# Kernel optimization log

Measured on AMD Instinct MI355X. Metric: run time of the kernel, lower is better.

The kernel has to match this reference:

```python
import jax, jax.numpy as jnp
import numpy as np

BETA = 8.0  # cfg.memory.beta (inverse temperature)
EPS = 1e-12  # matches F.normalize default eps


def _l2_normalize(x):
    return x / jnp.maximum(jnp.linalg.norm(x, axis=-1, keepdims=True), EPS)


def setup_inputs() -> dict:
    key = jax.random.key(0)
    k1, k2, k3 = jax.random.split(key, 3)
    embeddings = jax.random.normal(k1, (1024, 128), dtype=jnp.float32)   # queries [B, D]
    keys = jax.random.normal(k2, (100000, 128), dtype=jnp.float32)       # stored patterns [N, D]
    labels = jax.random.randint(k3, (100000,), 0, 1000)                  # class per stored pattern [N]
    return {"embeddings": embeddings, "keys": keys, "labels": labels, "n_classes": 1000}


def reference(embeddings, keys, labels, n_classes):
    # store(): keys normalized (normalize_keys=True); values = one_hot(labels)
    k = _l2_normalize(keys)
    # query(): normalize queries, cosine sims, softmax(beta*sims), weighted value sum
    q = _l2_normalize(embeddings)
    sims = q @ k.T                                   # [B, N]
    weights = jax.nn.softmax(BETA * sims, axis=-1)   # [B, N]
    # weights @ one_hot(labels, C) == segment-sum of weights by key label (same math,
    # avoids materializing the dense [N, C] one-hot value matrix)
    out = jax.ops.segment_sum(weights.T, labels, num_segments=n_classes).T  # [B, C]
    return out
```

## Files before the change

kernel.cpp:

```cpp
#include <hip/hip_runtime.h>
#include <math.h>

typedef _Float16 f16;
typedef _Float16 f16x8 __attribute__((ext_vector_type(8)));
typedef float    f32x16 __attribute__((ext_vector_type(16)));
typedef unsigned int uint;
typedef unsigned short u16;

#define B_Q     1024
#define DIM     128
#define N_KEYS  100000
#define NPAD    102400
#define NGP     (NPAD / 32)
#define GPC     8
#define NCHUNK  (NGP / GPC)
#define N_CLS   1000
#define QSCALE  11.541560327111707f
#define NH      128
#define QGRP    (B_Q / 32)

__global__ void k_hist(const int* __restrict__ labels, uint* __restrict__ hist128) {
    __shared__ uint lh[N_CLS];
    for (int i = threadIdx.x; i < N_CLS; i += blockDim.x) lh[i] = 0;
    __syncthreads();
    const int stride = gridDim.x * blockDim.x;
    for (int i = blockIdx.x * blockDim.x + threadIdx.x; i < N_KEYS; i += stride)
        atomicAdd(&lh[labels[i]], 1u);
    __syncthreads();
    for (int i = threadIdx.x; i < N_CLS; i += blockDim.x)
        hist128[blockIdx.x * N_CLS + i] = lh[i];
}

__global__ void k_scan(const uint* __restrict__ hist128, uint* __restrict__ cursor) {
    __shared__ uint s[1024];
    const int t = threadIdx.x;
    uint v = 0;
    if (t < N_CLS)
        for (int b = 0; b < NH; ++b) v += hist128[b * N_CLS + t];
    s[t] = v; __syncthreads();
    for (int o = 1; o < 1024; o <<= 1) {
        const uint x = (t >= o) ? s[t - o] : 0u;
        __syncthreads();
        s[t] += x;
        __syncthreads();
    }
    if (t < N_CLS) cursor[t] = s[t] - v;
}

__global__ void k_perm(const int* __restrict__ labels, uint* __restrict__ cursor,
                       int* __restrict__ src, u16* __restrict__ kcls) {
    const int n = blockIdx.x * blockDim.x + threadIdx.x;
    if (n >= NPAD) return;
    if (n < N_KEYS) {
        const int lab = labels[n];
        const int pos = (int)atomicAdd(&cursor[lab], 1u);
        src[pos]  = n;
        kcls[pos] = (u16)lab;
    } else {
        src[n]  = -1;
        kcls[n] = (u16)N_CLS;
    }
}

__global__ __launch_bounds__(256)
void k_gather(const float* __restrict__ qm, const float* __restrict__ km,
              const int* __restrict__ src, f16* __restrict__ kf2,
              f16* __restrict__ qf2) {
    __shared__ float ssq[8][32];
    __shared__ float scale[32];
    const int g = blockIdx.x;
    const int t = threadIdx.x;
    const int r = t & 31;
    const int p = t >> 5;
    const bool isq = g >= NGP;

    const float* srow;
    if (isq) srow = qm + (size_t)((g - NGP) * 32 + r) * DIM;
    else {
        const int sr = src[g * 32 + r];
        srow = (sr >= 0) ? km + (size_t)sr * DIM : nullptr;
    }

    float4 v[4];
    float ss = 0.0f;
    if (srow) {
        #pragma unroll
        for (int i = 0; i < 4; ++i) {
            v[i] = *(const float4*)(srow + p * 16 + i * 4);
            ss += v[i].x * v[i].x + v[i].y * v[i].y
                + v[i].z * v[i].z + v[i].w * v[i].w;
        }
    } else {
        #pragma unroll
        for (int i = 0; i < 4; ++i) v[i] = float4{0.f, 0.f, 0.f, 0.f};
    }
    ssq[p][r] = ss;
    __syncthreads();
    if (t < 32) {
        float s = 0.0f;
        #pragma unroll
        for (int i = 0; i < 8; ++i) s += ssq[i][t];
        scale[t] = (isq ? QSCALE : 1.0f) / fmaxf(sqrtf(s), 1e-12f);
    }
    __syncthreads();
    const float sc = scale[r];

    const float f[16] = {v[0].x, v[0].y, v[0].z, v[0].w,
                         v[1].x, v[1].y, v[1].z, v[1].w,
                         v[2].x, v[2].y, v[2].z, v[2].w,
                         v[3].x, v[3].y, v[3].z, v[3].w};
    f16x8 h0, h1;
    #pragma unroll
    for (int j = 0; j < 8; ++j) {
        h0[j] = (f16)(f[j]     * sc);
        h1[j] = (f16)(f[j + 8] * sc);
    }
    f16* dst = isq ? qf2 + (size_t)(g - NGP) * 4096
                   : kf2 + (size_t)g * 4096;
    *(f16x8*)(dst + p * 512 +       r * 8) = h0;
    *(f16x8*)(dst + p * 512 + 256 + r * 8) = h1;
}

#define ZFLOATS ((N_CLS + 2) * B_Q)
__global__ void k_meta(const u16* __restrict__ kcls, int* __restrict__ meta,
                       float* __restrict__ out_t) {
    const int nt = gridDim.x * blockDim.x;
    const float4 z = {0.0f, 0.0f, 0.0f, 0.0f};
    for (int i = blockIdx.x * blockDim.x + threadIdx.x; i < ZFLOATS / 4; i += nt)
        ((float4*)out_t)[i] = z;

    const int gid  = blockIdx.x * blockDim.x + threadIdx.x;
    const int g    = gid >> 6;
    const int lane = threadIdx.x & 63;
    if (g >= NGP) return;
    const int  cl = kcls[g * 32 + (lane & 31)];
    const int  ca = __shfl(cl, 0);
    const uint dm = (uint)(__ballot(cl != ca) & 0xffffffffull);
    const int  split = dm ? (__ffs(dm) - 1) : 32;
    const int  cb = (split < 32) ? __shfl(cl, split) : ca;
    if (lane == 0) meta[g] = ca | (cb << 11) | (split << 22);
}

#define FLUSH2(C) {                                                           \
        const float v0 = racc0 + __shfl_xor(racc0, 32);                       \
        const float v1 = racc1 + __shfl_xor(racc1, 32);                       \
        if ((C) != N_CLS) { tot0 += racc0; tot1 += racc1; }                   \
        if (lhi == 0) {                                                       \
            atomicAdd(&out_t[(size_t)(C) * B_Q + q00 + l31], v0);             \
            atomicAdd(&out_t[(size_t)(C) * B_Q + q01 + l31], v1);             \
        }                                                                     \
    }

#define LOADK(DST, I) {                                                       \
        const f16* _kb = kf2 + (size_t)(g0 + (I)) * 4096 + lane * 8;          \
        _Pragma("unroll")                                                     \
        for (int kk = 0; kk < 8; ++kk) DST[kk] = *(const f16x8*)(_kb + kk * 512); \
    }

#define BODY(KB, I) {                                                         \
        const int m     = __shfl(mv, (I));       \
        const int ca    = m & 0x7FF;                                          \
        const int cb    = (m >> 11) & 0x7FF;                                  \
        const int split = m >> 22;                                            \
        f32x16 c0 = {}, c1 = {};                                              \
        _Pragma("unroll")                                                     \
        for (int kk = 0; kk < 8; ++kk) {                                      \
            c0 = __builtin_amdgcn_mfma_f32_32x32x16_f16(KB[kk], Q0[kk], c0, 0, 0, 0); \
            c1 = __builtin_amdgcn_mfma_f32_32x32x16_f16(KB[kk], Q1[kk], c1, 0, 0, 0); \
        }                                                                     \
        if (ca != cur) {                                                      \
            if (cur >= 0) FLUSH2(cur);                                        \
            racc0 = 0.0f; racc1 = 0.0f;                                       \
            cur = ca;                                                         \
        }                                                                     \
        if (split == 32) {                                                    \
            float ga = 0.f, gb = 0.f, gc = 0.f, gd = 0.f;                     \
            _Pragma("unroll")                                                 \
            for (int r = 0; r < 16; r += 2) {                                 \
                ga += __builtin_amdgcn_exp2f(c0[r]);                          \
                gb += __builtin_amdgcn_exp2f(c0[r + 1]);                      \
                gc += __builtin_amdgcn_exp2f(c1[r]);                          \
                gd += __builtin_amdgcn_exp2f(c1[r + 1]);                      \
            }                                                                 \
            racc0 += ga + gb;                                                 \
            racc1 += gc + gd;                                                 \
        } else {                                                              \
            float ga = 0.f, gb = 0.f, gc = 0.f, gd = 0.f;                     \
            float ha = 0.f, hb = 0.f, hc = 0.f, hd = 0.f;                     \
            _Pragma("unroll")                                                 \
            for (int r = 0; r < 16; r += 2) {                                 \
                const int  kr0 = ((r & 3) + 8 * (r >> 2)) + lhi4;             \
                const int  kr1 = (((r + 1) & 3) + 8 * ((r + 1) >> 2)) + lhi4; \
                const float e0  = __builtin_amdgcn_exp2f(c0[r]);              \
                const float e0b = __builtin_amdgcn_exp2f(c0[r + 1]);          \
                const float e1  = __builtin_amdgcn_exp2f(c1[r]);              \
                const float e1b = __builtin_amdgcn_exp2f(c1[r + 1]);          \
                const bool inA0 = kr0 < split;                                \
                const bool inA1 = kr1 < split;                                \
                ga += inA0 ? e0  : 0.0f;  ha += inA0 ? 0.0f : e0;             \
                gb += inA1 ? e0b : 0.0f;  hb += inA1 ? 0.0f : e0b;            \
                gc += inA0 ? e1  : 0.0f;  hc += inA0 ? 0.0f : e1;             \
                gd += inA1 ? e1b : 0.0f;  hd += inA1 ? 0.0f : e1b;            \
            }                                                                 \
            racc0 += ga + gb;                                                 \
            racc1 += gc + gd;                                                 \
            FLUSH2(cur);                                                      \
            racc0 = ha + hb;                                                  \
            racc1 = hc + hd;                                                  \
            cur = cb;                                                         \
        }                                                                     \
    }

__global__ __launch_bounds__(64)
void class_gemm7(const f16* __restrict__ kf2, const f16* __restrict__ qf2,
                 const int* __restrict__ meta, float* __restrict__ out_t,
                 float* __restrict__ qtot) {
    const int lane = threadIdx.x & 63;
    const int l31  = lane & 31;
    const int lhi  = lane >> 5;
    const int lhi4 = lhi << 2;

    const int b     = blockIdx.x;
    const int xcd   = b & 7;
    const int u     = b >> 3;
    const int chunk = xcd * (NCHUNK / 8) + (u >> 4);
    const int qquad = (u >> 2) & 3;
    const int wsub  = u & 3;
    const int g0    = chunk * GPC;

    f16x8 Q0[8], Q1[8];
    {
        const f16* qa = qf2 + (size_t)(qquad * 8 + wsub * 2) * 4096 + lane * 8;
        #pragma unroll
        for (int kk = 0; kk < 8; ++kk) {
            Q0[kk] = *(const f16x8*)(qa + kk * 512);
            Q1[kk] = *(const f16x8*)(qa + 4096 + kk * 512);
        }
    }
    const int q00 = qquad * 256 + wsub * 64;
    const int q01 = q00 + 32;

    const int mv = meta[g0 + (lane & (GPC - 1))];

    float racc0 = 0.0f, racc1 = 0.0f;
    float tot0  = 0.0f, tot1  = 0.0f;
    int cur = -1;

    f16x8 K0[8], K1[8];
    LOADK(K0, 0);
    #pragma unroll
    for (int ii = 0; ii < GPC / 2; ++ii) {
        { const int i = 2 * ii;     if (i + 1 < GPC) LOADK(K1, i + 1); BODY(K0, i); }
        { const int i = 2 * ii + 1; if (i + 1 < GPC) LOADK(K0, i + 1); BODY(K1, i); }
    }
    if (cur >= 0) FLUSH2(cur);

    {
        const float t0 = tot0 + __shfl_xor(tot0, 32);
        const float t1 = tot1 + __shfl_xor(tot1, 32);
        if (lhi == 0) {
            atomicAdd(&qtot[q00 + l31], t0);
            atomicAdd(&qtot[q01 + l31], t1);
        }
    }
}

__global__ __launch_bounds__(256)
void k_norm_t(const float* __restrict__ out_t, const float* __restrict__ qtot,
              float* __restrict__ out) {
    __shared__ float tile[64 * 65];
    __shared__ float invq[64];
    const int tid  = threadIdx.x;
    const int w    = tid >> 6;
    const int lane = tid & 63;
    const int q0   = blockIdx.x * 64;
    const int c0   = blockIdx.y * 64;

    if (tid < 64) invq[tid] = 1.0f / qtot[q0 + tid];

    #pragma unroll
    for (int i = 0; i < 16; ++i) {
        const int cidx = c0 + w * 16 + i;
        const float v = (cidx < N_CLS) ? out_t[(size_t)cidx * B_Q + q0 + lane] : 0.0f;
        tile[lane * 65 + w * 16 + i] = v;
    }
    __syncthreads();
    #pragma unroll
    for (int j = 0; j < 16; ++j) {
        const int r    = w * 16 + j;
        const int cidx = c0 + lane;
        if (cidx < N_CLS)
            out[(size_t)(q0 + r) * N_CLS + cidx] = tile[r * 65 + lane] * invq[r];
    }
}

extern "C" void kernel_launch(void* const* d_in, const int* in_sizes, int n_in,
                              void* d_out, int out_size, void* d_ws, size_t ws_size,
                              hipStream_t stream) {
    const float* qm     = (const float*)d_in[0];
    const float* km     = (const float*)d_in[1];
    const int*   labels = (const int*)d_in[2];
    float* out = (float*)d_out;

    char* p = (char*)d_ws;
    f16*   kf2     = (f16*)p;   p += (size_t)NPAD * DIM * 2;
    f16*   qf2     = (f16*)p;   p += (size_t)B_Q * DIM * 2;
    float* out_t   = (float*)p; p += (size_t)N_CLS * B_Q * 4;
    float* sink    = (float*)p; p += (size_t)B_Q * 4;
    float* qtot    = (float*)p; p += (size_t)B_Q * 4;
    uint*  cursor  = (uint*)p;  p += N_CLS * 4;
    u16*   kcls    = (u16*)p;   p += (size_t)NPAD * 2;
    int*   meta    = (int*)p;   p += (size_t)NGP * 4;
    int*   src     = (int*)p;   p += (size_t)NPAD * 4;
    (void)sink;
    uint*  hist128 = (uint*)out_t;

    hipLaunchKernelGGL(k_hist, dim3(NH), dim3(256), 0, stream, labels, hist128);
    hipLaunchKernelGGL(k_scan, dim3(1), dim3(1024), 0, stream, hist128, cursor);
    hipLaunchKernelGGL(k_perm, dim3(NPAD / 256), dim3(256), 0, stream,
                       labels, cursor, src, kcls);
    hipLaunchKernelGGL(k_gather, dim3(NGP + QGRP), dim3(256), 0, stream,
                       qm, km, src, kf2, qf2);
    hipLaunchKernelGGL(k_meta, dim3((NGP * 64 + 255) / 256), dim3(256), 0, stream,
                       kcls, meta, out_t);

    hipLaunchKernelGGL(class_gemm7, dim3(16 * NCHUNK), dim3(64), 0, stream,
                       kf2, qf2, meta, out_t, qtot);

    hipLaunchKernelGGL(k_norm_t, dim3(B_Q / 64, (N_CLS + 63) / 64), dim3(256), 0, stream,
                       out_t, qtot, out);
}
```

Before: 101.6 us.

## Fuse meta/zeroing into gather, wave-shuffle scan, and double GPC per block

Removes the separate k_meta launch by folding output zeroing and per-group class metadata computation into k_gather. Rewrites the single-block scan to use wave-level shuffle prefix sums instead of a shared-memory Hillis-Steele loop with many barriers. Doubles key groups per GEMM block (halving grid size) and switches the main loop to non-unrolled, reducing launch overhead and meta reloads at the cost of less parallelism and a possibly weaker software pipeline.

```diff
diff --git a/kernel.cpp b/kernel.cpp
--- a/kernel.cpp
+++ b/kernel.cpp
@@ -12,12 +12,13 @@
 #define N_KEYS  100000
 #define NPAD    102400
 #define NGP     (NPAD / 32)
-#define GPC     8
+#define GPC     16
 #define NCHUNK  (NGP / GPC)
 #define N_CLS   1000
 #define QSCALE  11.541560327111707f
 #define NH      128
 #define QGRP    (B_Q / 32)
+#define ZFLOATS ((N_CLS + 2) * B_Q)
 
 __global__ void k_hist(const int* __restrict__ labels, uint* __restrict__ hist128) {
     __shared__ uint lh[N_CLS];
@@ -31,20 +32,34 @@
         hist128[blockIdx.x * N_CLS + i] = lh[i];
 }
 
-__global__ void k_scan(const uint* __restrict__ hist128, uint* __restrict__ cursor) {
-    __shared__ uint s[1024];
+__global__ __launch_bounds__(1024)
+void k_scan(const uint* __restrict__ hist128, uint* __restrict__ cursor) {
+    __shared__ uint wtot[16];
     const int t = threadIdx.x;
+    const int w = t >> 6, lane = t & 63;
     uint v = 0;
     if (t < N_CLS)
         for (int b = 0; b < NH; ++b) v += hist128[b * N_CLS + t];
-    s[t] = v; __syncthreads();
-    for (int o = 1; o < 1024; o <<= 1) {
-        const uint x = (t >= o) ? s[t - o] : 0u;
-        __syncthreads();
-        s[t] += x;
-        __syncthreads();
-    }
-    if (t < N_CLS) cursor[t] = s[t] - v;
+    uint s = v;
+    #pragma unroll
+    for (int o = 1; o < 64; o <<= 1) {
+        const uint x = __shfl_up(s, o);
+        if (lane >= o) s += x;
+    }
+    if (lane == 63) wtot[w] = s;
+    __syncthreads();
+    if (w == 0) {
+        uint ws = (lane < 16) ? wtot[lane] : 0;
+        #pragma unroll
+        for (int o = 1; o < 16; o <<= 1) {
+            const uint x = __shfl_up(ws, o);
+            if (lane >= o) ws += x;
+        }
+        if (lane < 16) wtot[lane] = ws;
+    }
+    __syncthreads();
+    const uint prefix = (w > 0) ? wtot[w - 1] : 0;
+    if (t < N_CLS) cursor[t] = prefix + s - v;
 }
 
 __global__ void k_perm(const int* __restrict__ labels, uint* __restrict__ cursor,
@@ -64,8 +79,9 @@
 
 __global__ __launch_bounds__(256)
 void k_gather(const float* __restrict__ qm, const float* __restrict__ km,
-              const int* __restrict__ src, f16* __restrict__ kf2,
-              f16* __restrict__ qf2) {
+              const int* __restrict__ src, const u16* __restrict__ kcls,
+              f16* __restrict__ kf2, f16* __restrict__ qf2,
+              int* __restrict__ meta, float* __restrict__ zbase) {
     __shared__ float ssq[8][32];
     __shared__ float scale[32];
     const int g = blockIdx.x;
@@ -73,6 +89,21 @@
     const int r = t & 31;
     const int p = t >> 5;
     const bool isq = g >= NGP;
+
+    {
+        const int zi = g * 256 + t;
+        if (zi < ZFLOATS / 4)
+            ((float4*)zbase)[zi] = float4{0.f, 0.f, 0.f, 0.f};
+    }
+
+    if (!isq && t < 64) {
+        const int  cl = kcls[g * 32 + (t & 31)];
+        const int  ca = __shfl(cl, 0);
+        const uint dm = (uint)(__ballot(cl != ca) & 0xffffffffull);
+        const int  split = dm ? (__ffs(dm) - 1) : 32;
+        const int  cb = (split < 32) ? __shfl(cl, split) : ca;
+        if (t == 0) meta[g] = ca | (cb << 11) | (split << 22);
+    }
 
     const float* srow;
     if (isq) srow = qm + (size_t)((g - NGP) * 32 + r) * DIM;
@@ -121,26 +152,6 @@
     *(f16x8*)(dst + p * 512 + 256 + r * 8) = h1;
 }
 
-#define ZFLOATS ((N_CLS + 2) * B_Q)
-__global__ void k_meta(const u16* __restrict__ kcls, int* __restrict__ meta,
-                       float* __restrict__ out_t) {
-    const int nt = gridDim.x * blockDim.x;
-    const float4 z = {0.0f, 0.0f, 0.0f, 0.0f};
-    for (int i = blockIdx.x * blockDim.x + threadIdx.x; i < ZFLOATS / 4; i += nt)
-        ((float4*)out_t)[i] = z;
-
-    const int gid  = blockIdx.x * blockDim.x + threadIdx.x;
-    const int g    = gid >> 6;
-    const int lane = threadIdx.x & 63;
-    if (g >= NGP) return;
-    const int  cl = kcls[g * 32 + (lane & 31)];
-    const int  ca = __shfl(cl, 0);
-    const uint dm = (uint)(__ballot(cl != ca) & 0xffffffffull);
-    const int  split = dm ? (__ffs(dm) - 1) : 32;
-    const int  cb = (split < 32) ? __shfl(cl, split) : ca;
-    if (lane == 0) meta[g] = ca | (cb << 11) | (split << 22);
-}
-
 #define FLUSH2(C) {                                                           \
         const float v0 = racc0 + __shfl_xor(racc0, 32);                       \
         const float v1 = racc1 + __shfl_xor(racc1, 32);                       \
@@ -158,7 +169,7 @@
     }
 
 #define BODY(KB, I) {                                                         \
-        const int m     = __shfl(mv, (I));       \
+        const int m     = __shfl(mv, (I));                                    \
         const int ca    = m & 0x7FF;                                          \
         const int cb    = (m >> 11) & 0x7FF;                                  \
         const int split = m >> 22;                                            \
@@ -212,7 +223,7 @@
     }
 
 __global__ __launch_bounds__(64)
-void class_gemm7(const f16* __restrict__ kf2, const f16* __restrict__ qf2,
+void class_gemm8(const f16* __restrict__ kf2, const f16* __restrict__ qf2,
                  const int* __restrict__ meta, float* __restrict__ out_t,
                  float* __restrict__ qtot) {
     const int lane = threadIdx.x & 63;
@@ -240,7 +251,7 @@
     const int q00 = qquad * 256 + wsub * 64;
     const int q01 = q00 + 32;
 
-    const int mv = meta[g0 + (lane & (GPC - 1))];
+    const int mv = meta[g0 + (lane & 15)];
 
     float racc0 = 0.0f, racc1 = 0.0f;
     float tot0  = 0.0f, tot1  = 0.0f;
@@ -248,10 +259,13 @@
 
     f16x8 K0[8], K1[8];
     LOADK(K0, 0);
-    #pragma unroll
+    #pragma unroll 1
     for (int ii = 0; ii < GPC / 2; ++ii) {
-        { const int i = 2 * ii;     if (i + 1 < GPC) LOADK(K1, i + 1); BODY(K0, i); }
-        { const int i = 2 * ii + 1; if (i + 1 < GPC) LOADK(K0, i + 1); BODY(K1, i); }
+        const int i0 = 2 * ii, i1 = 2 * ii + 1;
+        LOADK(K1, i1);
+        BODY(K0, i0);
+        if (ii + 1 < GPC / 2) LOADK(K0, i1 + 1);
+        BODY(K1, i1);
     }
     if (cur >= 0) FLUSH2(cur);
 
@@ -320,11 +334,9 @@
     hipLaunchKernelGGL(k_perm, dim3(NPAD / 256), dim3(256), 0, stream,
                        labels, cursor, src, kcls);
     hipLaunchKernelGGL(k_gather, dim3(NGP + QGRP), dim3(256), 0, stream,
-                       qm, km, src, kf2, qf2);
-    hipLaunchKernelGGL(k_meta, dim3((NGP * 64 + 255) / 256), dim3(256), 0, stream,
-                       kcls, meta, out_t);
-
-    hipLaunchKernelGGL(class_gemm7, dim3(16 * NCHUNK), dim3(64), 0, stream,
+                       qm, km, src, kcls, kf2, qf2, meta, out_t);
+
+    hipLaunchKernelGGL(class_gemm8, dim3(16 * NCHUNK), dim3(64), 0, stream,
                        kf2, qf2, meta, out_t, qtot);
 
     hipLaunchKernelGGL(k_norm_t, dim3(B_Q / 64, (N_CLS + 63) / 64), dim3(256), 0, stream,
```

New measurement: 103.0 us. About the same (+1.4%).
